# Optimization experiments

Measured on AMD Instinct MI355X. Metric: run time of the kernel, lower is better.

Reference implementation:

```python
import jax, jax.numpy as jnp
import numpy as np

B, T, C = 16, 8192, 256
E, K = 8, 2
CAPACITY = int(T / E * 1.25)  # 1280, per (row, expert) token capacity
DFF = 4 * C


def setup_inputs() -> dict:
    key = jax.random.key(0)
    ks = jax.random.split(key, 8)
    s = 0.02
    return {
        "x": jax.random.normal(ks[0], (B, T, C), jnp.float32),
        "rW1": jax.random.normal(ks[1], (C, DFF), jnp.float32) * s,
        "rb1": jnp.zeros((DFF,), jnp.float32),
        "rW2": jax.random.normal(ks[2], (DFF, DFF), jnp.float32) * s,
        "rb2": jnp.zeros((DFF,), jnp.float32),
        "rW3": jax.random.normal(ks[3], (DFF, E), jnp.float32) * s,
        "rb3": jnp.zeros((E,), jnp.float32),
        "eWi": jax.random.normal(ks[4], (E, C, DFF), jnp.float32) * s,
        "ebi": jnp.zeros((E, DFF), jnp.float32),
        "eWo": jax.random.normal(ks[5], (E, DFF, C), jnp.float32) * s,
        "ebo": jnp.zeros((E, C), jnp.float32),
    }


def _row_kept_mask(cnt):
    # Mask over per-row token *ranks*: which of the cnt routed tokens survive capacity.
    # Over capacity: torch.linspace(0, cnt-1, CAPACITY).int() subsampling.
    cnt_f = cnt.astype(jnp.float32)
    lin = jnp.floor(jnp.arange(CAPACITY, dtype=jnp.float32) * (cnt_f - 1.0) / (CAPACITY - 1)).astype(jnp.int32)
    m_lin = jnp.zeros((T,), bool).at[jnp.clip(lin, 0, T - 1)].set(True)
    m_all = jnp.arange(T) < cnt
    return jnp.where(cnt > CAPACITY, m_lin, m_all)


def reference(x, rW1, rb1, rW2, rb2, rW3, rb3, eWi, ebi, eWo, ebo):
    # Router MLP (dropout = identity in eval) + softmax
    h = jax.nn.relu(x @ rW1 + rb1)
    h = jax.nn.relu(h @ rW2 + rb2)
    probs = jax.nn.softmax(h @ rW3 + rb3, axis=-1)          # [B,T,E]
    topk_probs, topk_experts = jax.lax.top_k(probs, K)      # [B,T,K]

    out = jnp.zeros_like(x)
    rows = jnp.arange(B)[:, None]
    for e in range(E):
        sel_k = topk_experts == e                            # [B,T,K]
        sel = sel_k.any(-1)                                  # [B,T] token routed to e
        w = (topk_probs * sel_k).sum(-1)                     # [B,T] gate weight
        count = sel.sum(-1)                                  # [B]
        rank = jnp.cumsum(sel, axis=1) - 1                   # [B,T] rank within row (t-sorted)
        kept_by_rank = jax.vmap(_row_kept_mask)(count)       # [B,T]
        kept = sel & jnp.take_along_axis(kept_by_rank, jnp.clip(rank, 0, T - 1), axis=1)
        # gather up to CAPACITY kept tokens per row (stable keeps t order)
        idx = jnp.argsort(~kept, axis=1, stable=True)[:, :CAPACITY]       # [B,cap]
        valid = jnp.take_along_axis(kept, idx, axis=1)                    # [B,cap]
        toks = jnp.take_along_axis(x, idx[..., None], axis=1)             # [B,cap,C]
        y = jax.nn.relu(toks @ eWi[e] + ebi[e]) @ eWo[e] + ebo[e]         # expert FFN
        gate = valid * jnp.take_along_axis(w, idx, axis=1)                # [B,cap]
        out = out.at[rows, idx].add(y * gate[..., None])
    return out


if __name__ == "__main__":
    print(reference(**setup_inputs()).shape)
```

## Files before the change

### kernel.cpp

```cpp
#include <hip/hip_runtime.h>
#include <hip/hip_bf16.h>
#include <stdint.h>

namespace {

constexpr int TT    = 8192;
constexpr int BB    = 16;
constexpr int CD    = 256;
constexpr int FD    = 1024;
constexpr int CAPY  = 1280;
constexpr int NTOK  = BB * TT;
constexpr int NPAIR = BB * 8;
constexpr int FLAGCAP1 = 16384;
constexpr int FLAGCAP2 = 4096;
constexpr int TPC   = 32768;
constexpr int NCHUNK = NTOK / TPC;

using f4 = float4;
typedef __attribute__((ext_vector_type(8))) short short8;
typedef __attribute__((ext_vector_type(8))) _Float16 half8;
typedef __attribute__((ext_vector_type(4))) float f32x4;

#define MFMA_BF __builtin_amdgcn_mfma_f32_16x16x32_bf16
#define MFMA_HF __builtin_amdgcn_mfma_f32_16x16x32_f16

__device__ __forceinline__ f4 ld4(const float* p){ return *(const f4*)p; }

__device__ __forceinline__ unsigned short bfh(float x){
  uint32_t u = __float_as_uint(x);
  return (unsigned short)((u + 0x7fffu + ((u >> 16) & 1u)) >> 16);
}
__device__ __forceinline__ float b2f(unsigned short h){
  return __uint_as_float(((uint32_t)h) << 16);
}
__device__ __forceinline__ uint32_t packbf(float x){
  uint32_t u = __float_as_uint(x);
  uint32_t hi = (u + 0x7fffu + ((u >> 16) & 1u)) & 0xffff0000u;
  float r = x - __uint_as_float(hi);
  uint32_t v = __float_as_uint(r);
  uint32_t lo = ((v + 0x7fffu + ((v >> 16) & 1u)) >> 16) & 0xffffu;
  return hi | lo;
}
__device__ __forceinline__ unsigned short f16b(float v){
  union { _Float16 h; unsigned short u; } U; U.h = (_Float16)v; return U.u;
}
__device__ __forceinline__ void unpack8(const uint32_t* p, short8& h, short8& l){
  uint4 a = *(const uint4*)p;
  uint4 b = *(const uint4*)(p + 4);
  union { uint32_t u[4]; short8 s; } H, L;
  H.u[0] = (a.y & 0xffff0000u) | (a.x >> 16);  L.u[0] = (a.y << 16) | (a.x & 0xffffu);
  H.u[1] = (a.w & 0xffff0000u) | (a.z >> 16);  L.u[1] = (a.w << 16) | (a.z & 0xffffu);
  H.u[2] = (b.y & 0xffff0000u) | (b.x >> 16);  L.u[2] = (b.y << 16) | (b.x & 0xffffu);
  H.u[3] = (b.w & 0xffff0000u) | (b.z >> 16);  L.u[3] = (b.w << 16) | (b.z & 0xffffu);
  h = H.s; l = L.s;
}

__device__ __forceinline__ void gload16(const unsigned short* g, unsigned short* l){
  __builtin_amdgcn_global_load_lds(
      (const __attribute__((address_space(1))) void*)reinterpret_cast<uintptr_t>(g),
      (__attribute__((address_space(3))) void*)(uint32_t)reinterpret_cast<uintptr_t>(l),
      16, 0, 0);
}

__global__ __launch_bounds__(256)
void x_to_f16(const float* __restrict__ x, unsigned short* __restrict__ o)
{
  const size_t i = (size_t)blockIdx.x*256 + threadIdx.x;
  const float* p = x + i*16;
  f4 a = ld4(p), b = ld4(p+4), c = ld4(p+8), d = ld4(p+12);
  union { unsigned short u[16]; uint4 q[2]; } U;
  U.u[0]=f16b(a.x); U.u[1]=f16b(a.y); U.u[2]=f16b(a.z); U.u[3]=f16b(a.w);
  U.u[4]=f16b(b.x); U.u[5]=f16b(b.y); U.u[6]=f16b(b.z); U.u[7]=f16b(b.w);
  U.u[8]=f16b(c.x); U.u[9]=f16b(c.y); U.u[10]=f16b(c.z); U.u[11]=f16b(c.w);
  U.u[12]=f16b(d.x);U.u[13]=f16b(d.y);U.u[14]=f16b(d.z); U.u[15]=f16b(d.w);
  *(uint4*)(o + i*16)     = U.q[0];
  *(uint4*)(o + i*16 + 8) = U.q[1];
}

__global__ __launch_bounds__(256)
void prep_transpose(const float* __restrict__ in, unsigned short* __restrict__ oh,
                    unsigned short* __restrict__ ol, int R, int C)
{
  __shared__ float T[32][33];
  const int tx = threadIdx.x & 31, ty = threadIdx.x >> 5;
  const size_t bs = (size_t)R * C;
  const float* ib = in + bs * blockIdx.z;
  unsigned short* ohb = oh + bs * blockIdx.z;
  unsigned short* olb = ol + bs * blockIdx.z;
  const int r0 = blockIdx.y * 32, c0 = blockIdx.x * 32;
  #pragma unroll
  for (int j = 0; j < 4; ++j)
    T[ty + 8*j][tx] = ib[(size_t)(r0 + ty + 8*j)*C + c0 + tx];
  __syncthreads();
  #pragma unroll
  for (int j = 0; j < 4; ++j){
    float v = T[tx][ty + 8*j];
    unsigned short h = bfh(v);
    unsigned short lo = bfh(v - b2f(h));
    size_t o = (size_t)(c0 + ty + 8*j)*R + r0 + tx;
    ohb[o] = h; olb[o] = lo;
  }
}

__global__ __launch_bounds__(256)
void prep_transpose_f16(const float* __restrict__ in, unsigned short* __restrict__ o, int R, int C)
{
  __shared__ float T[32][33];
  const int tx = threadIdx.x & 31, ty = threadIdx.x >> 5;
  const size_t bs = (size_t)R * C;
  const float* ib = in + bs * blockIdx.z;
  unsigned short* ob = o + bs * blockIdx.z;
  const int r0 = blockIdx.y * 32, c0 = blockIdx.x * 32;
  #pragma unroll
  for (int j = 0; j < 4; ++j)
    T[ty + 8*j][tx] = ib[(size_t)(r0 + ty + 8*j)*C + c0 + tx];
  __syncthreads();
  #pragma unroll
  for (int j = 0; j < 4; ++j)
    ob[(size_t)(c0 + ty + 8*j)*R + r0 + tx] = f16b(T[tx][ty + 8*j]);
}

__global__ __launch_bounds__(256, 2)
void gemm_a(const unsigned short* __restrict__ xF, int tok0,
            const unsigned short* __restrict__ W1F,
            const float* __restrict__ b1,
            unsigned short* __restrict__ H1)
{
  __shared__ unsigned short smem[16384];
  unsigned short* As = smem;
  unsigned short* Bs = smem + 8192;
  const int tid = threadIdx.x;
  const int w = tid >> 6, lane = tid & 63, l15 = lane & 15, l4 = lane >> 4;
  const int wm = w >> 1, wn = w & 1;
  const int bid = ((int)blockIdx.x & 7) * ((int)gridDim.x >> 3) + ((int)blockIdx.x >> 3);
  const int mt0 = (bid >> 3) * 128;
  const int nt0 = (bid & 7) * 128;
  const int row_s = tid >> 1, half = tid & 1;
  const int lrow = lane >> 3;
  const int srcAB = lrow*CD + (((lane & 7) ^ lrow) << 3);

  f32x4 acc[4][4];
  #pragma unroll
  for (int mt = 0; mt < 4; ++mt)
    #pragma unroll
    for (int nt = 0; nt < 4; ++nt)
      acc[mt][nt] = (f32x4){0.f,0.f,0.f,0.f};

  #pragma unroll 1
  for (int ks = 0; ks < 4; ++ks){
    const unsigned short* abase = xF  + (size_t)(tok0 + mt0)*CD + ks*64;
    const unsigned short* bbase = W1F + (size_t)nt0*CD + ks*64;
    #pragma unroll
    for (int i = 0; i < 4; ++i){
      const int r0 = w*32 + i*8;
      gload16(abase + (size_t)r0*CD + srcAB, As + r0*64);
      gload16(bbase + (size_t)r0*CD + srcAB, Bs + r0*64);
    }
    __syncthreads();
    #pragma unroll
    for (int kt = 0; kt < 2; ++kt){
      half8 af[4], bf[4];
      #pragma unroll
      for (int mt = 0; mt < 4; ++mt){
        const int r = 64*wm + 16*mt + l15;
        af[mt] = *(const half8*)&As[r*64 + (((kt*4 + l4) ^ (r & 7)) << 3)];
      }
      #pragma unroll
      for (int nt = 0; nt < 4; ++nt){
        const int r = 64*wn + 16*nt + l15;
        bf[nt] = *(const half8*)&Bs[r*64 + (((kt*4 + l4) ^ (r & 7)) << 3)];
      }
      #pragma unroll
      for (int mt = 0; mt < 4; ++mt)
        #pragma unroll
        for (int nt = 0; nt < 4; ++nt)
          acc[mt][nt] = MFMA_HF(af[mt], bf[nt], acc[mt][nt], 0,0,0);
    }
    __syncthreads();
  }

  unsigned short* Cs = smem;
  #pragma unroll
  for (int nt = 0; nt < 4; ++nt){
    const int ncol = 64*wn + 16*nt + l15;
    const float b1v = b1[nt0 + ncol];
    #pragma unroll
    for (int mt = 0; mt < 4; ++mt)
      #pragma unroll
      for (int r = 0; r < 4; ++r){
        const int tr = 64*wm + 16*mt + 4*l4 + r;
        Cs[tr*128 + ncol] = f16b(fmaxf(acc[mt][nt][r] + b1v, 0.f));
      }
  }
  __syncthreads();
  {
    unsigned short* dst = H1 + (size_t)(mt0 + row_s)*FD + nt0 + half*64;
    const unsigned short* src = Cs + row_s*128 + half*64;
    #pragma unroll
    for (int j = 0; j < 8; ++j) ((uint4*)dst)[j] = ((const uint4*)src)[j];
  }
}

__global__ __launch_bounds__(256, 2)
void gemm_b(const unsigned short* __restrict__ H1, int tok0,
            const unsigned short* __restrict__ W2F,
            const float* __restrict__ b2,
            const float* __restrict__ W3,
            float* __restrict__ plg)
{
  __shared__ unsigned short smem[16384];
  unsigned short* As = smem;
  unsigned short* Bs = smem + 8192;
  const int tid = threadIdx.x;
  const int w = tid >> 6, lane = tid & 63, l15 = lane & 15, l4 = lane >> 4;
  const int wm = w >> 1, wn = w & 1;
  const int bid = ((int)blockIdx.x & 7) * ((int)gridDim.x >> 3) + ((int)blockIdx.x >> 3);
  const int ntile = bid & 7;
  const int mt0 = (bid >> 3) * 128;
  const int nt0 = ntile * 128;
  const int row_s = tid >> 1, half = tid & 1;
  const int lrow = lane >> 3;
  const int srcAB = lrow*FD + (((lane & 7) ^ lrow) << 3);

  f32x4 acc[4][4];
  #pragma unroll
  for (int mt = 0; mt < 4; ++mt)
    #pragma unroll
    for (int nt = 0; nt < 4; ++nt)
      acc[mt][nt] = (f32x4){0.f,0.f,0.f,0.f};

  #pragma unroll 1
  for (int ks = 0; ks < 16; ++ks){
    const unsigned short* abase = H1  + (size_t)mt0*FD + ks*64;
    const unsigned short* bbase = W2F + (size_t)nt0*FD + ks*64;
    #pragma unroll
    for (int i = 0; i < 4; ++i){
      const int r0 = w*32 + i*8;
      gload16(abase + (size_t)r0*FD + srcAB, As + r0*64);
      gload16(bbase + (size_t)r0*FD + srcAB, Bs + r0*64);
    }
    __syncthreads();
    #pragma unroll
    for (int kt = 0; kt < 2; ++kt){
      half8 af[4], bf[4];
      #pragma unroll
      for (int mt = 0; mt < 4; ++mt){
        const int r = 64*wm + 16*mt + l15;
        af[mt] = *(const half8*)&As[r*64 + (((kt*4 + l4) ^ (r & 7)) << 3)];
      }
      #pragma unroll
      for (int nt = 0; nt < 4; ++nt){
        const int r = 64*wn + 16*nt + l15;
        bf[nt] = *(const half8*)&Bs[r*64 + (((kt*4 + l4) ^ (r & 7)) << 3)];
      }
      #pragma unroll
      for (int mt = 0; mt < 4; ++mt)
        #pragma unroll
        for (int nt = 0; nt < 4; ++nt)
          acc[mt][nt] = MFMA_HF(af[mt], bf[nt], acc[mt][nt], 0,0,0);
    }
    __syncthreads();
  }

  float* lgs = (float*)smem;
  *(f4*)&lgs[tid*4] = (f4){0.f,0.f,0.f,0.f};
  __syncthreads();

  #pragma unroll
  for (int mt = 0; mt < 4; ++mt){
    float lp[4][8];
    #pragma unroll
    for (int r = 0; r < 4; ++r)
      #pragma unroll
      for (int e = 0; e < 8; ++e) lp[r][e] = 0.f;
    #pragma unroll
    for (int nt = 0; nt < 4; ++nt){
      const int n2 = nt0 + 64*wn + 16*nt + l15;
      const float b2v = b2[n2];
      f4 wa = ld4(W3 + n2*8), wb3 = ld4(W3 + n2*8 + 4);
      const float w3s[8] = {wa.x,wa.y,wa.z,wa.w,wb3.x,wb3.y,wb3.z,wb3.w};
      #pragma unroll
      for (int r = 0; r < 4; ++r){
        float h2 = fmaxf(acc[mt][nt][r] + b2v, 0.f);
        #pragma unroll
        for (int e = 0; e < 8; ++e)
          lp[r][e] = fmaf(h2, w3s[e], lp[r][e]);
      }
    }
    #pragma unroll
    for (int off = 1; off < 16; off <<= 1)
      #pragma unroll
      for (int r = 0; r < 4; ++r)
        #pragma unroll
        for (int e = 0; e < 8; ++e)
          lp[r][e] += __shfl_xor(lp[r][e], off);
    if (l15 == 0){
      #pragma unroll
      for (int r = 0; r < 4; ++r){
        const int row = 64*wm + 16*mt + 4*l4 + r;
        #pragma unroll
        for (int e = 0; e < 8; ++e)
          atomicAdd(&lgs[row*8 + e], lp[r][e]);
      }
    }
  }
  __syncthreads();
  {
    f4 v = *(const f4*)&lgs[row_s*8 + half*4];
    *(f4*)(plg + ((size_t)ntile*NTOK + tok0 + mt0 + row_s)*8 + half*4) = v;
  }
}

__global__ __launch_bounds__(256)
void top2_kernel(const float* __restrict__ plg, const float* __restrict__ b3,
                 int2* __restrict__ topE, float2* __restrict__ topW,
                 int* __restrict__ flagList, int* __restrict__ flagCnt)
{
  const int tok = blockIdx.x*256 + threadIdx.x;
  float l[8];
  #pragma unroll
  for (int e = 0; e < 8; ++e) l[e] = b3[e];
  #pragma unroll
  for (int s = 0; s < 8; ++s){
    const float* p = plg + ((size_t)s*NTOK + tok)*8;
    f4 p0 = ld4(p), p1 = ld4(p + 4);
    l[0]+=p0.x; l[1]+=p0.y; l[2]+=p0.z; l[3]+=p0.w;
    l[4]+=p1.x; l[5]+=p1.y; l[6]+=p1.z; l[7]+=p1.w;
  }
  int e1 = 0; float v1 = l[0];
  #pragma unroll
  for (int e = 1; e < 8; ++e){ if (l[e] > v1){ v1 = l[e]; e1 = e; } }
  int e2 = 0; float v2 = -3.0e38f;
  #pragma unroll
  for (int e = 0; e < 8; ++e){ if (e != e1 && l[e] > v2){ v2 = l[e]; e2 = e; } }
  float v3 = -3.0e38f;
  #pragma unroll
  for (int e = 0; e < 8; ++e){ if (e != e1 && e != e2 && l[e] > v3) v3 = l[e]; }
  float s = 0.f;
  #pragma unroll
  for (int e = 0; e < 8; ++e) s += expf(l[e]-v1);
  topE[tok] = make_int2(e1, e2);
  topW[tok] = make_float2(1.0f/s, expf(v2 - v1)/s);
  if (v2 - v3 < 5e-4f){
    int i = atomicAdd(flagCnt, 1);
    if (i < FLAGCAP1) flagList[i] = tok;
  }
}

__global__ __launch_bounds__(512, 2)
void router_fix1(const float* __restrict__ x,
                 const unsigned short* __restrict__ W1Th, const unsigned short* __restrict__ W1Tl,
                 const float* __restrict__ b1,
                 const unsigned short* __restrict__ W2Th, const unsigned short* __restrict__ W2Tl,
                 const float* __restrict__ b2,
                 const float* __restrict__ W3, const float* __restrict__ b3,
                 const int* __restrict__ flagList, const int* __restrict__ flagCnt,
                 int2* __restrict__ topE, float2* __restrict__ topW,
                 int* __restrict__ flagList2, int* __restrict__ flagCnt2)
{
  int cnt = *flagCnt; if (cnt > FLAGCAP1) cnt = FLAGCAP1;
  const int s0 = blockIdx.x * 32;
  if (s0 >= cnt) return;

  __shared__ uint32_t Xp[32*256];
  __shared__ uint32_t Hp[32*128];
  __shared__ float lgs[32*8];
  __shared__ int sTok[32];
  const int tid = threadIdx.x;
  const int w = tid >> 6, lane = tid & 63;
  const int l15 = lane & 15, l4 = lane >> 4;
  const int swz = l15 & 7;

  if (tid < 32){
    const int s = s0 + tid;
    sTok[tid] = (s < cnt) ? flagList[s] : flagList[s0];
  }
  if (tid < 256) lgs[tid] = 0.f;
  __syncthreads();
  {
    const int row = tid >> 4, cb = (tid & 15) * 2;
    const float* rp = x + (size_t)sTok[row]*CD + cb*8;
    #pragma unroll
    for (int g = 0; g < 2; ++g){
      f4 a = ld4(rp + g*8), bq = ld4(rp + g*8 + 4);
      uint32_t* dst = &Xp[row*256 + (((cb + g) ^ (row & 7)) << 3)];
      *(uint4*)dst     = make_uint4(packbf(a.x),packbf(a.y),packbf(a.z),packbf(a.w));
      *(uint4*)(dst+4) = make_uint4(packbf(bq.x),packbf(bq.y),packbf(bq.z),packbf(bq.w));
    }
  }
  __syncthreads();

  f32x4 acc2[2][8];
  #pragma unroll
  for (int mt = 0; mt < 2; ++mt)
    #pragma unroll
    for (int nt = 0; nt < 8; ++nt)
      acc2[mt][nt] = (f32x4){0.f,0.f,0.f,0.f};

  #pragma unroll 1
  for (int kc = 0; kc < 8; ++kc){
    f32x4 acc1[2] = {(f32x4){0,0,0,0},(f32x4){0,0,0,0}};
    const int n1g = kc*128 + 16*w + l15;
    const size_t wb1 = (size_t)n1g * 256;
    #pragma unroll
    for (int kt = 0; kt < 8; ++kt){
      short8 ah[2], al[2];
      #pragma unroll
      for (int mt = 0; mt < 2; ++mt)
        unpack8(&Xp[(mt*16 + l15)*256 + ((((kt<<2) + l4) ^ swz) << 3)], ah[mt], al[mt]);
      const int kb = kt*32 + 8*l4;
      short8 bh = *(const short8*)&W1Th[wb1 + kb];
      short8 bl = *(const short8*)&W1Tl[wb1 + kb];
      #pragma unroll
      for (int mt = 0; mt < 2; ++mt)
        acc1[mt] = MFMA_BF(ah[mt], bh, MFMA_BF(ah[mt], bl, MFMA_BF(al[mt], bh, acc1[mt],0,0,0),0,0,0),0,0,0);
    }
    __syncthreads();
    {
      const float b1v = b1[n1g];
      const int c = 16*w + l15, ch = c >> 3, co = c & 7;
      #pragma unroll
      for (int mt = 0; mt < 2; ++mt)
        #pragma unroll
        for (int r = 0; r < 4; ++r){
          const int row = mt*16 + 4*l4 + r;
          Hp[row*128 + ((ch ^ (row & 7)) << 3) + co] = packbf(fmaxf(acc1[mt][r] + b1v, 0.f));
        }
    }
    __syncthreads();
    #pragma unroll
    for (int kt = 0; kt < 4; ++kt){
      short8 ah[2], al[2];
      #pragma unroll
      for (int mt = 0; mt < 2; ++mt)
        unpack8(&Hp[(mt*16 + l15)*128 + ((((kt<<2) + l4) ^ swz) << 3)], ah[mt], al[mt]);
      const size_t kg = (size_t)(kc*128 + kt*32 + 8*l4);
      #pragma unroll
      for (int nt = 0; nt < 8; ++nt){
        const size_t wb2 = (size_t)(128*w + 16*nt + l15) * 1024 + kg;
        short8 bh = *(const short8*)&W2Th[wb2];
        short8 bl = *(const short8*)&W2Tl[wb2];
        #pragma unroll
        for (int mt = 0; mt < 2; ++mt)
          acc2[mt][nt] = MFMA_BF(ah[mt], bh, MFMA_BF(ah[mt], bl, MFMA_BF(al[mt], bh, acc2[mt][nt],0,0,0),0,0,0),0,0,0);
      }
    }
  }

  #pragma unroll
  for (int mt = 0; mt < 2; ++mt){
    float lp[4][8];
    #pragma unroll
    for (int r = 0; r < 4; ++r)
      #pragma unroll
      for (int e = 0; e < 8; ++e) lp[r][e] = 0.f;
    #pragma unroll
    for (int nt = 0; nt < 8; ++nt){
      const int n2 = 128*w + 16*nt + l15;
      const float b2v = b2[n2];
      f4 wa = ld4(W3 + n2*8), wb3 = ld4(W3 + n2*8 + 4);
      const float w3s[8] = {wa.x,wa.y,wa.z,wa.w,wb3.x,wb3.y,wb3.z,wb3.w};
      #pragma unroll
      for (int r = 0; r < 4; ++r){
        float h2 = fmaxf(acc2[mt][nt][r] + b2v, 0.f);
        #pragma unroll
        for (int e = 0; e < 8; ++e)
          lp[r][e] = fmaf(h2, w3s[e], lp[r][e]);
      }
    }
    #pragma unroll
    for (int off = 1; off < 16; off <<= 1)
      #pragma unroll
      for (int r = 0; r < 4; ++r)
        #pragma unroll
        for (int e = 0; e < 8; ++e)
          lp[r][e] += __shfl_xor(lp[r][e], off);
    if (l15 == 0){
      #pragma unroll
      for (int r = 0; r < 4; ++r){
        const int row = mt*16 + 4*l4 + r;
        #pragma unroll
        for (int e = 0; e < 8; ++e)
          atomicAdd(&lgs[row*8 + e], lp[r][e]);
      }
    }
  }
  __syncthreads();

  if (tid < 32 && s0 + tid < cnt){
    const int tok = sTok[tid];
    float l[8];
    #pragma unroll
    for (int e = 0; e < 8; ++e) l[e] = lgs[tid*8 + e] + b3[e];
    int e1 = 0; float v1 = l[0];
    #pragma unroll
    for (int e = 1; e < 8; ++e){ if (l[e] > v1){ v1 = l[e]; e1 = e; } }
    int e2 = 0; float v2 = -3.0e38f;
    #pragma unroll
    for (int e = 0; e < 8; ++e){ if (e != e1 && l[e] > v2){ v2 = l[e]; e2 = e; } }
    float v3 = -3.0e38f;
    #pragma unroll
    for (int e = 0; e < 8; ++e){ if (e != e1 && e != e2 && l[e] > v3) v3 = l[e]; }
    float s = 0.f;
    #pragma unroll
    for (int e = 0; e < 8; ++e) s += expf(l[e]-v1);
    topE[tok] = make_int2(e1, e2);
    topW[tok] = make_float2(1.0f/s, expf(v2 - v1)/s);
    if (v2 - v3 < 1e-4f){
      int i = atomicAdd(flagCnt2, 1);
      if (i < FLAGCAP2) flagList2[i] = tok;
    }
  }
}

__global__ __launch_bounds__(256)
void router_fixup(const float* __restrict__ x,
                  const float* __restrict__ W1, const float* __restrict__ b1,
                  const float* __restrict__ W2, const float* __restrict__ b2,
                  const float* __restrict__ W3, const float* __restrict__ b3,
                  const int* __restrict__ flagList, const int* __restrict__ flagCnt,
                  int2* __restrict__ topE, float2* __restrict__ topW)
{
  int n = *flagCnt; if (n > FLAGCAP2) n = FLAGCAP2;
  if ((int)blockIdx.x >= n) return;
  const int t = flagList[blockIdx.x];
  __shared__ float xs[256];
  __shared__ float h1[1024];
  __shared__ float h2[1024];
  __shared__ float lgf[8];
  const int tid = threadIdx.x;
  xs[tid] = x[(size_t)t*256 + tid];
  __syncthreads();
  {
    float a0=b1[tid], a1=b1[tid+256], a2=b1[tid+512], a3=b1[tid+768];
    for (int k = 0; k < 256; ++k){
      const float xv = xs[k];
      const float* wr = W1 + (size_t)k*1024;
      a0 = fmaf(xv, wr[tid],     a0);
      a1 = fmaf(xv, wr[tid+256], a1);
      a2 = fmaf(xv, wr[tid+512], a2);
      a3 = fmaf(xv, wr[tid+768], a3);
    }
    h1[tid]=fmaxf(a0,0.f); h1[tid+256]=fmaxf(a1,0.f); h1[tid+512]=fmaxf(a2,0.f); h1[tid+768]=fmaxf(a3,0.f);
  }
  __syncthreads();
  {
    float a0=b2[tid], a1=b2[tid+256], a2=b2[tid+512], a3=b2[tid+768];
    for (int k = 0; k < 1024; ++k){
      const float hv = h1[k];
      const float* wr = W2 + (size_t)k*1024;
      a0 = fmaf(hv, wr[tid],     a0);
      a1 = fmaf(hv, wr[tid+256], a1);
      a2 = fmaf(hv, wr[tid+512], a2);
      a3 = fmaf(hv, wr[tid+768], a3);
    }
    h2[tid]=fmaxf(a0,0.f); h2[tid+256]=fmaxf(a1,0.f); h2[tid+512]=fmaxf(a2,0.f); h2[tid+768]=fmaxf(a3,0.f);
  }
  __syncthreads();
  {
    const int e = tid >> 5, s = tid & 31;
    float p = 0.f;
    for (int k = s*32; k < s*32+32; ++k) p = fmaf(h2[k], W3[(size_t)k*8 + e], p);
    #pragma unroll
    for (int off = 1; off < 32; off <<= 1) p += __shfl_xor(p, off);
    if (s == 0) lgf[e] = p + b3[e];
  }
  __syncthreads();
  if (tid == 0){
    float l[8];
    #pragma unroll
    for (int e=0;e<8;++e) l[e] = lgf[e];
    int e1 = 0; float v1 = l[0];
    #pragma unroll
    for (int e=1;e<8;++e){ if (l[e] > v1){ v1 = l[e]; e1 = e; } }
    int e2 = 0; float v2 = -3.0e38f;
    #pragma unroll
    for (int e=0;e<8;++e){ if (e != e1 && l[e] > v2){ v2 = l[e]; e2 = e; } }
    float s = 0.f;
    #pragma unroll
    for (int e=0;e<8;++e) s += expf(l[e]-v1);
    topE[t] = make_int2(e1, e2);
    topW[t] = make_float2(1.0f/s, expf(v2 - v1)/s);
  }
}

__global__ __launch_bounds__(256)
void route_compact(const int2* __restrict__ topE, const float2* __restrict__ topW,
                   int* __restrict__ listIdx, float* __restrict__ listW, int* __restrict__ kcnt)
{
  const int blk = blockIdx.x;
  const int b = blk >> 3, e = blk & 7;
  const int2* te = topE + (size_t)b*TT;
  const float2* tw = topW + (size_t)b*TT;
  __shared__ unsigned kmask[256];
  __shared__ int wTot[4], wTot2[4];
  __shared__ int s_cnt, s_baseRank, s_baseSlot;
  const int tid = threadIdx.x;
  const int lane = tid & 63, wid = tid >> 6;

  if (tid == 0){ s_cnt = 0; s_baseRank = 0; s_baseSlot = 0; }
  kmask[tid & 255] = 0;
  __syncthreads();

  int c = 0;
  for (int t = tid; t < TT; t += 256){
    int2 v = te[t];
    c += (v.x == e) || (v.y == e);
  }
  #pragma unroll
  for (int off = 32; off; off >>= 1) c += __shfl_xor(c, off);
  if (lane == 0) atomicAdd(&s_cnt, c);
  __syncthreads();
  const int cnt = s_cnt;

  if (cnt > CAPY){
    for (int i = tid; i < CAPY; i += 256){
      float t1 = (float)i * (float)(cnt - 1);
      float t2 = t1 / 1279.0f;
      int r = (int)floorf(t2);
      atomicOr(&kmask[r >> 5], 1u << (r & 31));
    }
  }
  __syncthreads();

  for (int tile = 0; tile < 32; ++tile){
    const int t = tile*256 + tid;
    const int2 v = te[t];
    const bool sel = (v.x == e) || (v.y == e);
    const float2 wv = tw[t];
    const float w = (v.x == e) ? wv.x : wv.y;

    unsigned long long mSel = __ballot(sel);
    const int lpfx = __popcll(mSel & ((1ull << lane) - 1ull));
    if (lane == 0) wTot[wid] = __popcll(mSel);
    __syncthreads();
    int wpfx = 0;
    for (int wdx = 0; wdx < wid; ++wdx) wpfx += wTot[wdx];
    const int rank = s_baseRank + wpfx + lpfx;

    const bool kept = sel && (cnt <= CAPY || ((kmask[rank >> 5] >> (rank & 31)) & 1u));
    unsigned long long mK = __ballot(kept);
    const int lpfx2 = __popcll(mK & ((1ull << lane) - 1ull));
    if (lane == 0) wTot2[wid] = __popcll(mK);
    __syncthreads();
    int wpfx2 = 0;
    for (int wdx = 0; wdx < wid; ++wdx) wpfx2 += wTot2[wdx];
    const int slot = s_baseSlot + wpfx2 + lpfx2;

    if (kept){
      listIdx[(size_t)blk*CAPY + slot] = t;
      listW [(size_t)blk*CAPY + slot] = w;
    }
    __syncthreads();
    if (tid == 0){
      int a = 0, q = 0;
      for (int wdx = 0; wdx < 4; ++wdx){ a += wTot[wdx]; q += wTot2[wdx]; }
      s_baseRank += a; s_baseSlot += q;
    }
    __syncthreads();
  }
  if (tid == 0) kcnt[blk] = s_baseSlot;
}

__global__ __launch_bounds__(512, 3)
void expert_mfma(const float* __restrict__ x,
                 const unsigned short* __restrict__ WiF, const float* __restrict__ ebi,
                 const unsigned short* __restrict__ WoF, const float* __restrict__ ebo,
                 const int* __restrict__ listIdx, const float* __restrict__ listW,
                 const int* __restrict__ kcnt, float* __restrict__ out)
{
  const int q = blockIdx.y;
  const int e = q >> 4, b = q & 15;
  const int pair = b*8 + e;
  const int kc_n = kcnt[pair];
  const int s0 = blockIdx.x * 64;
  if (s0 >= kc_n) return;

  __shared__ unsigned short Xf[64*256];
  __shared__ unsigned short Hf[64*128];
  __shared__ int sTok[64];
  __shared__ float sG[64];
  const int tid = threadIdx.x;
  const int w = tid >> 6, lane = tid & 63;
  const int l15 = lane & 15, l4 = lane >> 4;
  const int swz = l15 & 7;

  if (tid < 64){
    const int s = s0 + tid;
    const bool v = s < kc_n;
    sTok[tid] = v ? listIdx[(size_t)pair*CAPY + s] : -1;
    sG[tid]   = v ? listW [(size_t)pair*CAPY + s] : 0.f;
  }
  __syncthreads();
  {
    const int row = tid >> 3, cb = (tid & 7) * 4;
    int tk = sTok[row]; if (tk < 0) tk = 0;
    const float* rp = x + ((size_t)b*TT + tk)*CD + cb*8;
    #pragma unroll
    for (int g = 0; g < 4; ++g){
      f4 a = ld4(rp + g*8), bq = ld4(rp + g*8 + 4);
      union { unsigned short u[8]; short8 s; } U;
      U.u[0]=f16b(a.x); U.u[1]=f16b(a.y); U.u[2]=f16b(a.z); U.u[3]=f16b(a.w);
      U.u[4]=f16b(bq.x);U.u[5]=f16b(bq.y);U.u[6]=f16b(bq.z);U.u[7]=f16b(bq.w);
      *(short8*)&Xf[row*256 + (((cb + g) ^ (row & 7)) << 3)] = U.s;
    }
  }
  __syncthreads();

  const unsigned short* Wi = WiF + (size_t)e*FD*CD;
  const unsigned short* Wo = WoF + (size_t)e*CD*FD;

  f32x4 accO[4][2];
  #pragma unroll
  for (int mt = 0; mt < 4; ++mt)
    #pragma unroll
    for (int nt = 0; nt < 2; ++nt)
      accO[mt][nt] = (f32x4){0.f,0.f,0.f,0.f};

  #pragma unroll 1
  for (int kc = 0; kc < 8; ++kc){
    f32x4 acc1[4] = {(f32x4){0,0,0,0},(f32x4){0,0,0,0},(f32x4){0,0,0,0},(f32x4){0,0,0,0}};
    const int n1g = kc*128 + 16*w + l15;
    const size_t wbi = (size_t)n1g * 256;
    #pragma unroll
    for (int kt = 0; kt < 8; ++kt){
      half8 av[4];
      #pragma unroll
      for (int mt = 0; mt < 4; ++mt)
        av[mt] = *(const half8*)&Xf[(mt*16 + l15)*256 + ((((kt<<2) + l4) ^ swz) << 3)];
      half8 bf = *(const half8*)&Wi[wbi + kt*32 + 8*l4];
      #pragma unroll
      for (int mt = 0; mt < 4; ++mt)
        acc1[mt] = MFMA_HF(av[mt], bf, acc1[mt], 0,0,0);
    }
    __syncthreads();
    {
      const float biv = ebi[e*FD + n1g];
      const int c = 16*w + l15, ch = c >> 3, co = c & 7;
      #pragma unroll
      for (int mt = 0; mt < 4; ++mt)
        #pragma unroll
        for (int r = 0; r < 4; ++r){
          const int row = mt*16 + 4*l4 + r;
          Hf[row*128 + ((ch ^ (row & 7)) << 3) + co] = f16b(fmaxf(acc1[mt][r] + biv, 0.f));
        }
    }
    __syncthreads();
    #pragma unroll
    for (int kt = 0; kt < 4; ++kt){
      half8 av[4];
      #pragma unroll
      for (int mt = 0; mt < 4; ++mt)
        av[mt] = *(const half8*)&Hf[(mt*16 + l15)*128 + ((((kt<<2) + l4) ^ swz) << 3)];
      const size_t kg = (size_t)(kc*128 + kt*32 + 8*l4);
      #pragma unroll
      for (int nt = 0; nt < 2; ++nt){
        const int n = 32*w + 16*nt + l15;
        half8 bf = *(const half8*)&Wo[(size_t)n*1024 + kg];
        #pragma unroll
        for (int mt = 0; mt < 4; ++mt)
          accO[mt][nt] = MFMA_HF(av[mt], bf, accO[mt][nt], 0,0,0);
      }
    }
  }

  #pragma unroll
  for (int mt = 0; mt < 4; ++mt)
    #pragma unroll
    for (int r = 0; r < 4; ++r){
      const int row = mt*16 + 4*l4 + r;
      const int tk = sTok[row];
      if (tk >= 0){
        const float g = sG[row];
        #pragma unroll
        for (int nt = 0; nt < 2; ++nt){
          const int n = 32*w + 16*nt + l15;
          atomicAdd(out + ((size_t)b*TT + tk)*CD + n, (accO[mt][nt][r] + ebo[e*CD + n]) * g);
        }
      }
    }
}

}

extern "C" void kernel_launch(void* const* d_in, const int* in_sizes, int n_in,
                              void* d_out, int out_size, void* d_ws, size_t ws_size,
                              hipStream_t stream)
{
  const float* x   = (const float*)d_in[0];
  const float* rW1 = (const float*)d_in[1];
  const float* rb1 = (const float*)d_in[2];
  const float* rW2 = (const float*)d_in[3];
  const float* rb2 = (const float*)d_in[4];
  const float* rW3 = (const float*)d_in[5];
  const float* rb3 = (const float*)d_in[6];
  const float* eWi = (const float*)d_in[7];
  const float* ebi = (const float*)d_in[8];
  const float* eWo = (const float*)d_in[9];
  const float* ebo = (const float*)d_in[10];
  (void)in_sizes; (void)n_in; (void)ws_size;

  char* ws = (char*)d_ws;
  size_t off = 0;
  auto carve = [&](size_t bytes)->char*{ char* p = ws + off; off += (bytes + 255) & ~(size_t)255; return p; };
  unsigned short* W1F  = (unsigned short*)carve((size_t)FD*CD*2);
  unsigned short* W2F  = (unsigned short*)carve((size_t)FD*FD*2);
  unsigned short* W1Th = (unsigned short*)carve((size_t)FD*CD*2);
  unsigned short* W1Tl = (unsigned short*)carve((size_t)FD*CD*2);
  unsigned short* W2Th = (unsigned short*)carve((size_t)FD*FD*2);
  unsigned short* W2Tl = (unsigned short*)carve((size_t)FD*FD*2);
  unsigned short* WiF  = (unsigned short*)carve((size_t)8*FD*CD*2);
  unsigned short* WoF  = (unsigned short*)carve((size_t)8*CD*FD*2);
  unsigned short* xF16 = (unsigned short*)carve((size_t)NTOK*CD*2);
  unsigned short* H1   = (unsigned short*)carve((size_t)TPC*FD*2);
  float*  plg     = (float*)carve((size_t)8*NTOK*8*sizeof(float));
  int2*   topE    = (int2*)carve((size_t)NTOK*sizeof(int2));
  float2* topW    = (float2*)carve((size_t)NTOK*sizeof(float2));
  int*    listIdx = (int*)carve((size_t)NPAIR*CAPY*sizeof(int));
  float*  listW   = (float*)carve((size_t)NPAIR*CAPY*sizeof(float));
  int*    kcnt    = (int*)carve((size_t)NPAIR*sizeof(int));
  int*    flagCnt = (int*)carve(256);
  int*    flagCnt2= (int*)carve(256);
  int*    flagList= (int*)carve((size_t)FLAGCAP1*sizeof(int));
  int*    flagList2=(int*)carve((size_t)FLAGCAP2*sizeof(int));

  float* out = (float*)d_out;
  hipMemsetAsync(out, 0, (size_t)out_size*sizeof(float), stream);
  hipMemsetAsync(flagCnt, 0, sizeof(int), stream);
  hipMemsetAsync(flagCnt2, 0, sizeof(int), stream);

  x_to_f16<<<NTOK*CD/16/256, 256, 0, stream>>>(x, xF16);
  prep_transpose_f16<<<dim3(32, 8, 1), 256, 0, stream>>>(rW1, W1F, 256, 1024);
  prep_transpose_f16<<<dim3(32,32, 1), 256, 0, stream>>>(rW2, W2F, 1024, 1024);
  prep_transpose<<<dim3(32, 8, 1), 256, 0, stream>>>(rW1, W1Th, W1Tl, 256, 1024);
  prep_transpose<<<dim3(32,32, 1), 256, 0, stream>>>(rW2, W2Th, W2Tl, 1024, 1024);
  prep_transpose_f16<<<dim3(32, 8, 8), 256, 0, stream>>>(eWi, WiF, 256, 1024);
  prep_transpose_f16<<<dim3( 8,32, 8), 256, 0, stream>>>(eWo, WoF, 1024, 256);

  for (int c = 0; c < NCHUNK; ++c){
    gemm_a<<<(TPC/128)*8, 256, 0, stream>>>(xF16, c*TPC, W1F, rb1, H1);
    gemm_b<<<(TPC/128)*8, 256, 0, stream>>>(H1, c*TPC, W2F, rb2, rW3, plg);
  }
  top2_kernel<<<NTOK/256, 256, 0, stream>>>(plg, rb3, topE, topW, flagList, flagCnt);

  router_fix1<<<FLAGCAP1/32, 512, 0, stream>>>(x, W1Th, W1Tl, rb1, W2Th, W2Tl, rb2,
                                               rW3, rb3, flagList, flagCnt,
                                               topE, topW, flagList2, flagCnt2);
  router_fixup<<<FLAGCAP2, 256, 0, stream>>>(x, rW1, rb1, rW2, rb2, rW3, rb3,
                                             flagList2, flagCnt2, topE, topW);
  route_compact<<<NPAIR, 256, 0, stream>>>(topE, topW, listIdx, listW, kcnt);
  expert_mfma<<<dim3(CAPY/64, 128), 512, 0, stream>>>(x, WiF, ebi, WoF, ebo,
                                                      listIdx, listW, kcnt, out);
}
```

Baseline: 1.326 ms.

## Double-buffer LDS tiles in router GEMMs to overlap loads with MFMA

Both router GEMM kernels (gemm_a and gemm_b) now use two LDS stages instead of one. A stage helper issues the next k-slice's global-to-LDS loads before the MFMA work on the current slice, so memory latency is meant to hide behind compute. In exchange, LDS per block doubles to 64KB, which may limit how many blocks fit on a CU. Correctness depends on the existing end-of-iteration barrier and the wait on the asynchronous loads.

```diff
diff --git a/kernel.cpp b/kernel.cpp
--- a/kernel.cpp
+++ b/kernel.cpp
@@ -126,9 +126,7 @@
             const float* __restrict__ b1,
             unsigned short* __restrict__ H1)
 {
-  __shared__ unsigned short smem[16384];
-  unsigned short* As = smem;
-  unsigned short* Bs = smem + 8192;
+  __shared__ unsigned short smem[32768];
   const int tid = threadIdx.x;
   const int w = tid >> 6, lane = tid & 63, l15 = lane & 15, l4 = lane >> 4;
   const int wm = w >> 1, wn = w & 1;
@@ -139,6 +137,19 @@
   const int lrow = lane >> 3;
   const int srcAB = lrow*CD + (((lane & 7) ^ lrow) << 3);
 
+  auto stage = [&](int buf, int ks){
+    const unsigned short* abase = xF  + (size_t)(tok0 + mt0)*CD + ks*64;
+    const unsigned short* bbase = W1F + (size_t)nt0*CD + ks*64;
+    unsigned short* As_ = smem + buf*16384;
+    unsigned short* Bs_ = As_ + 8192;
+    #pragma unroll
+    for (int i = 0; i < 4; ++i){
+      const int r0 = w*32 + i*8;
+      gload16(abase + (size_t)r0*CD + srcAB, As_ + r0*64);
+      gload16(bbase + (size_t)r0*CD + srcAB, Bs_ + r0*64);
+    }
+  };
+
   f32x4 acc[4][4];
   #pragma unroll
   for (int mt = 0; mt < 4; ++mt)
@@ -146,17 +157,15 @@
     for (int nt = 0; nt < 4; ++nt)
       acc[mt][nt] = (f32x4){0.f,0.f,0.f,0.f};
 
+  stage(0, 0);
+  __syncthreads();
+
   #pragma unroll 1
   for (int ks = 0; ks < 4; ++ks){
-    const unsigned short* abase = xF  + (size_t)(tok0 + mt0)*CD + ks*64;
-    const unsigned short* bbase = W1F + (size_t)nt0*CD + ks*64;
-    #pragma unroll
-    for (int i = 0; i < 4; ++i){
-      const int r0 = w*32 + i*8;
-      gload16(abase + (size_t)r0*CD + srcAB, As + r0*64);
-      gload16(bbase + (size_t)r0*CD + srcAB, Bs + r0*64);
-    }
-    __syncthreads();
+    const int cur = ks & 1;
+    if (ks + 1 < 4) stage(cur ^ 1, ks + 1);
+    const unsigned short* As = smem + cur*16384;
+    const unsigned short* Bs = As + 8192;
     #pragma unroll
     for (int kt = 0; kt < 2; ++kt){
       half8 af[4], bf[4];
@@ -208,9 +217,7 @@
             const float* __restrict__ W3,
             float* __restrict__ plg)
 {
-  __shared__ unsigned short smem[16384];
-  unsigned short* As = smem;
-  unsigned short* Bs = smem + 8192;
+  __shared__ unsigned short smem[32768];
   const int tid = threadIdx.x;
   const int w = tid >> 6, lane = tid & 63, l15 = lane & 15, l4 = lane >> 4;
   const int wm = w >> 1, wn = w & 1;
@@ -222,6 +229,19 @@
   const int lrow = lane >> 3;
   const int srcAB = lrow*FD + (((lane & 7) ^ lrow) << 3);
 
+  auto stage = [&](int buf, int ks){
+    const unsigned short* abase = H1  + (size_t)mt0*FD + ks*64;
+    const unsigned short* bbase = W2F + (size_t)nt0*FD + ks*64;
+    unsigned short* As_ = smem + buf*16384;
+    unsigned short* Bs_ = As_ + 8192;
+    #pragma unroll
+    for (int i = 0; i < 4; ++i){
+      const int r0 = w*32 + i*8;
+      gload16(abase + (size_t)r0*FD + srcAB, As_ + r0*64);
+      gload16(bbase + (size_t)r0*FD + srcAB, Bs_ + r0*64);
+    }
+  };
+
   f32x4 acc[4][4];
   #pragma unroll
   for (int mt = 0; mt < 4; ++mt)
@@ -229,17 +249,15 @@
     for (int nt = 0; nt < 4; ++nt)
       acc[mt][nt] = (f32x4){0.f,0.f,0.f,0.f};
 
+  stage(0, 0);
+  __syncthreads();
+
   #pragma unroll 1
   for (int ks = 0; ks < 16; ++ks){
-    const unsigned short* abase = H1  + (size_t)mt0*FD + ks*64;
-    const unsigned short* bbase = W2F + (size_t)nt0*FD + ks*64;
-    #pragma unroll
-    for (int i = 0; i < 4; ++i){
-      const int r0 = w*32 + i*8;
-      gload16(abase + (size_t)r0*FD + srcAB, As + r0*64);
-      gload16(bbase + (size_t)r0*FD + srcAB, Bs + r0*64);
-    }
-    __syncthreads();
+    const int cur = ks & 1;
+    if (ks + 1 < 16) stage(cur ^ 1, ks + 1);
+    const unsigned short* As = smem + cur*16384;
+    const unsigned short* Bs = As + 8192;
     #pragma unroll
     for (int kt = 0; kt < 2; ++kt){
       half8 af[4], bf[4];
```

Result: slower. 1.367 ms (+3.1%).
